# Performance work log

Measured on AMD Instinct MI355X. Metric: run time of the kernel, lower is better.

The kernel has to match this reference:

```python
import jax, jax.numpy as jnp
import numpy as np

K = 20  # kNN neighbours (conf.k)

def knn_edge_feats(x, k):
    """x: [B, C, N] -> edge features [B, 2C, N, k] (central || neighbor-central)."""
    xt = jnp.swapaxes(x, 1, 2)                       # [B, N, C]
    sq = jnp.sum(xt * xt, axis=2, keepdims=True)     # [B, N, 1]
    dist = -2.0 * jnp.einsum('bnc,bcm->bnm', xt, x) + sq + jnp.swapaxes(sq, 1, 2)  # [B,N,N]
    idx = jnp.argsort(dist, axis=2)[:, :, 1:k + 1]   # [B, N, k], skip self (col 0)
    nbrs = jax.vmap(lambda xb, ib: xb[:, ib])(x, idx)  # [B, C, N, k]
    central = x[:, :, :, None]                        # [B, C, N, 1]
    return jnp.concatenate([jnp.broadcast_to(central, nbrs.shape), nbrs - central], axis=1)

def edge_conv(x, w, b, k):
    """1x1 conv over edge features, max over k.  x:[B,C,N], w:[Fout,2C], b:[Fout]."""
    ee = knn_edge_feats(x, k)                                   # [B, 2C, N, k]
    y = jnp.einsum('oc,bcnk->bonk', w, ee) + b[None, :, None, None]
    return jnp.max(y, axis=3)                                   # [B, Fout, N]

def setup_inputs() -> dict:
    key = jax.random.key(0)
    ks = iter(jax.random.split(key, 32))
    B, N = 16, 2048
    d = {}
    d['x'] = jax.random.normal(next(ks), (B, 3, N), dtype=jnp.float32)
    def w(shape, scale):
        return jax.random.normal(next(ks), shape, dtype=jnp.float32) * scale
    d['ec0_w'] = w((64, 6), 0.3);    d['ec0_b'] = w((64,), 0.05)
    d['ec1_w'] = w((64, 128), 0.08); d['ec1_b'] = w((64,), 0.05)
    d['ec2_w'] = w((64, 128), 0.08); d['ec2_b'] = w((64,), 0.05)
    d['ec3_w'] = w((128, 128), 0.08); d['ec3_b'] = w((128,), 0.05)
    d['conv0_w'] = w((1024, 320), 0.05); d['conv0_b'] = w((1024,), 0.05)
    d['conv0_s'] = jax.random.uniform(next(ks), (1024,), minval=0.5, maxval=1.5)
    d['conv0_t'] = w((1024,), 0.05)
    d['fc0_w'] = w((512, 1024), 0.03); d['fc0_b'] = w((512,), 0.05)
    d['fc0_s'] = jax.random.uniform(next(ks), (512,), minval=0.5, maxval=1.5)
    d['fc0_t'] = w((512,), 0.05)
    d['fc1_w'] = w((256, 512), 0.04); d['fc1_b'] = w((256,), 0.05)
    d['fc1_s'] = jax.random.uniform(next(ks), (256,), minval=0.5, maxval=1.5)
    d['fc1_t'] = w((256,), 0.05)
    d['fc2_w'] = w((40, 256), 0.06); d['fc2_b'] = w((40,), 0.05)
    d['fc2_s'] = jax.random.uniform(next(ks), (40,), minval=0.5, maxval=1.5)
    d['fc2_t'] = w((40,), 0.05)
    return d

def reference(x, ec0_w, ec0_b, ec1_w, ec1_b, ec2_w, ec2_b, ec3_w, ec3_b,
              conv0_w, conv0_b, conv0_s, conv0_t,
              fc0_w, fc0_b, fc0_s, fc0_t,
              fc1_w, fc1_b, fc1_s, fc1_t,
              fc2_w, fc2_b, fc2_s, fc2_t):
    x1 = edge_conv(x, ec0_w, ec0_b, K)    # [B, 64, N]
    x2 = edge_conv(x1, ec1_w, ec1_b, K)   # [B, 64, N]
    x3 = edge_conv(x2, ec2_w, ec2_b, K)   # [B, 64, N]
    x4 = edge_conv(x3, ec3_w, ec3_b, K)   # [B, 128, N]
    h = jnp.concatenate([x1, x2, x3, x4], axis=1)              # [B, 320, N]
    # conv1dbr: 1x1 conv + BN(affine folded into s,t) + ReLU
    h = jnp.einsum('oc,bcn->bon', conv0_w, h) + conv0_b[None, :, None]
    h = jax.nn.relu(h * conv0_s[None, :, None] + conv0_t[None, :, None])  # [B, 1024, N]
    g = jnp.max(h, axis=2)                                     # [B, 1024]
    # fcbr blocks: linear + BN + ReLU
    g = jax.nn.relu((g @ fc0_w.T + fc0_b) * fc0_s + fc0_t)     # [B, 512]
    g = jax.nn.relu((g @ fc1_w.T + fc1_b) * fc1_s + fc1_t)     # [B, 256]
    g = jax.nn.relu((g @ fc2_w.T + fc2_b) * fc2_s + fc2_t)     # [B, 40]
    return g
```

## Files before the change

### kernel.cpp

```cpp
#include <hip/hip_runtime.h>

#define DEVINL __device__ __forceinline__

static const int NPTS = 2048;

typedef __attribute__((ext_vector_type(8))) short bf16x8;
typedef __attribute__((ext_vector_type(4))) float f32x4;

DEVINL unsigned fenc(float x) {
    int b = __float_as_int(x);
    return (b < 0) ? ~(unsigned)b : ((unsigned)b | 0x80000000u);
}
DEVINL float fdec(unsigned u) {
    return (u & 0x80000000u) ? __int_as_float((int)(u & 0x7fffffffu))
                             : __int_as_float((int)~u);
}
DEVINL unsigned long long u64min(unsigned long long a, unsigned long long b) {
    return (b < a) ? b : a;
}
DEVINL unsigned short f2bf(float x) {
    unsigned u = __float_as_uint(x);
    return (unsigned short)((u + 0x7fffu + ((u >> 16) & 1u)) >> 16);
}
DEVINL float bf2f(unsigned short h) { return __uint_as_float(((unsigned)h) << 16); }

DEVINL void topk20(float v[32], unsigned long long* cand, int lane,
                   int* __restrict__ Iout, int outBase) {
    float t16[16];
#pragma unroll
    for (int i = 0; i < 16; ++i) t16[i] = fminf(v[i], v[i + 16]);
#pragma unroll
    for (int i = 0; i < 8; ++i) t16[i] = fminf(t16[i], t16[i + 8]);
#pragma unroll
    for (int i = 0; i < 4; ++i) t16[i] = fminf(t16[i], t16[i + 4]);
    float s = fminf(fminf(t16[0], t16[1]), fminf(t16[2], t16[3]));
#pragma unroll
    for (int k = 2; k <= 64; k <<= 1) {
#pragma unroll
        for (int j = k >> 1; j >= 1; j >>= 1) {
            float o = __shfl_xor(s, j);
            bool keepmin = (((lane & j) == 0) == ((lane & k) == 0));
            s = keepmin ? fminf(s, o) : fmaxf(s, o);
        }
    }
    const float tau = __shfl(s, 19);
    int cnt = 0;
#pragma unroll
    for (int j = 0; j < 32; ++j) {
        bool pass = (v[j] <= tau);
        unsigned long long mask = __ballot(pass);
        if (pass) {
            int pos = cnt + (int)__popcll(mask & ((1ull << lane) - 1ull));
            if (pos < 64) {
                int col = lane * 4 + (j & 3) + ((j >> 2) << 8);
                cand[pos] = ((unsigned long long)fenc(v[j]) << 32) | (unsigned)col;
            }
        }
        cnt += (int)__popcll(mask);
    }
    if (cnt <= 64) {
        unsigned long long key = (lane < cnt) ? cand[lane] : ~0ull;
#pragma unroll
        for (int k = 2; k <= 64; k <<= 1) {
#pragma unroll
            for (int j = k >> 1; j >= 1; j >>= 1) {
                unsigned long long o = __shfl_xor(key, j);
                bool keepmin = (((lane & j) == 0) == ((lane & k) == 0));
                unsigned long long mn = u64min(key, o);
                unsigned long long mx = (key ^ o) ^ mn;
                key = keepmin ? mn : mx;
            }
        }
        if (lane < 20) Iout[outBase + lane] = (int)(unsigned)(key & 0xffffffffu);
    } else {
        unsigned long long vk[32];
#pragma unroll
        for (int j = 0; j < 32; ++j) {
            int col = lane * 4 + (j & 3) + ((j >> 2) << 8);
            vk[j] = ((unsigned long long)fenc(v[j]) << 32) | (unsigned)col;
        }
        unsigned long long last = 0ull;
        for (int it = 0; it < 20; ++it) {
            unsigned long long q16[16];
#pragma unroll
            for (int i = 0; i < 16; ++i) {
                unsigned long long a = (vk[i] > last) ? vk[i] : ~0ull;
                unsigned long long c = (vk[i + 16] > last) ? vk[i + 16] : ~0ull;
                q16[i] = u64min(a, c);
            }
#pragma unroll
            for (int i = 0; i < 8; ++i) q16[i] = u64min(q16[i], q16[i + 8]);
#pragma unroll
            for (int i = 0; i < 4; ++i) q16[i] = u64min(q16[i], q16[i + 4]);
            unsigned long long best = u64min(u64min(q16[0], q16[1]), u64min(q16[2], q16[3]));
#pragma unroll
            for (int off = 32; off >= 1; off >>= 1) {
                unsigned long long o = __shfl_down(best, off);
                best = u64min(best, o);
            }
            best = __shfl(best, 0);
            if (lane == 0) Iout[outBase + it] = (int)(unsigned)(best & 0xffffffffu);
            last = best;
        }
    }
}

__global__ __launch_bounds__(256) void sqmax_kernel(const float* __restrict__ X, int bs,
                                                    float* __restrict__ sqOut,
                                                    unsigned* __restrict__ Rsq) {
    const int N = NPTS;
    const int b = blockIdx.y, m = blockIdx.x * 256 + threadIdx.x;
    const float* __restrict__ Xb = X + (size_t)b * bs;
    float s = 0.f;
#pragma unroll 8
    for (int c = 0; c < 64; ++c) { float t = Xb[(size_t)c * N + m]; s = fmaf(t, t, s); }
    sqOut[(b << 11) + m] = s;
    float mx = s;
#pragma unroll
    for (int off = 32; off >= 1; off >>= 1) mx = fmaxf(mx, __shfl_down(mx, off));
    if ((threadIdx.x & 63) == 0) atomicMax(&Rsq[b], __float_as_uint(mx));
}

__global__ __launch_bounds__(512) void knnmfma_kernel(
    const unsigned short* __restrict__ HtH, const unsigned short* __restrict__ HtL,
    int hoff, const float* __restrict__ Xt,
    const float* __restrict__ sqB, const unsigned* __restrict__ Rsq,
    int* __restrict__ Iout) {
    extern __shared__ char smem[];
    float* Dr = (float*)smem;
    int* cand = (int*)(smem + 65792);
    const int N = NPTS, K = 20, DS = 1028;
    const int b = blockIdx.y, n0 = blockIdx.x * 16;
    const int tid = threadIdx.x, wave = tid >> 6, lane = tid & 63;
    const int fr = lane & 15, quad = lane >> 4;
    const float Rmax = sqrtf(__uint_as_float(Rsq[b]));

    const size_t abase = ((size_t)(b * N + n0 + fr)) * 320 + hoff + quad * 8;
    const bf16x8 aH0 = *(const bf16x8*)&HtH[abase];
    const bf16x8 aH1 = *(const bf16x8*)&HtH[abase + 32];
    const bf16x8 aL0 = *(const bf16x8*)&HtL[abase];
    const bf16x8 aL1 = *(const bf16x8*)&HtL[abase + 32];

    float v[2][2][16];
#pragma unroll
    for (int pass = 0; pass < 2; ++pass) {
#pragma unroll 2
        for (int tt = 0; tt < 8; ++tt) {
            const int m0 = pass * 1024 + wave * 128 + tt * 16;
            const size_t bbase = ((size_t)(b * N + m0 + fr)) * 320 + hoff + quad * 8;
            bf16x8 bH0 = *(const bf16x8*)&HtH[bbase];
            bf16x8 bH1 = *(const bf16x8*)&HtH[bbase + 32];
            bf16x8 bL0 = *(const bf16x8*)&HtL[bbase];
            bf16x8 bL1 = *(const bf16x8*)&HtL[bbase + 32];
            f32x4 acc = (f32x4){0.f, 0.f, 0.f, 0.f};
            acc = __builtin_amdgcn_mfma_f32_16x16x32_bf16(aH0, bH0, acc, 0, 0, 0);
            acc = __builtin_amdgcn_mfma_f32_16x16x32_bf16(aH1, bH1, acc, 0, 0, 0);
            acc = __builtin_amdgcn_mfma_f32_16x16x32_bf16(aH0, bL0, acc, 0, 0, 0);
            acc = __builtin_amdgcn_mfma_f32_16x16x32_bf16(aH1, bL1, acc, 0, 0, 0);
            acc = __builtin_amdgcn_mfma_f32_16x16x32_bf16(aL0, bH0, acc, 0, 0, 0);
            acc = __builtin_amdgcn_mfma_f32_16x16x32_bf16(aL1, bH1, acc, 0, 0, 0);
            const float sqv = sqB[(b << 11) + m0 + fr];
            const int mloc = wave * 128 + tt * 16 + fr;
#pragma unroll
            for (int r = 0; r < 4; ++r)
                Dr[(quad * 4 + r) * DS + mloc] = sqv - 2.f * acc[r];
        }
        __syncthreads();
#pragma unroll
        for (int rr = 0; rr < 2; ++rr) {
            const float* __restrict__ rp = &Dr[(wave * 2 + rr) * DS];
#pragma unroll
            for (int q = 0; q < 4; ++q) {
                float4 x4 = *(const float4*)&rp[lane * 4 + q * 256];
                v[pass][rr][q * 4 + 0] = x4.x; v[pass][rr][q * 4 + 1] = x4.y;
                v[pass][rr][q * 4 + 2] = x4.z; v[pass][rr][q * 4 + 3] = x4.w;
            }
        }
        __syncthreads();
    }

    int cntk[2];
#pragma unroll
    for (int rr = 0; rr < 2; ++rr) {
        const int nrow = n0 + wave * 2 + rr;
        float lm = v[0][rr][0];
#pragma unroll
        for (int j = 1; j < 16; ++j) lm = fminf(lm, v[0][rr][j]);
#pragma unroll
        for (int j = 0; j < 16; ++j) lm = fminf(lm, v[1][rr][j]);
        float s = lm;
#pragma unroll
        for (int k = 2; k <= 64; k <<= 1) {
#pragma unroll
            for (int j = k >> 1; j >= 1; j >>= 1) {
                float o = __shfl_xor(s, j);
                bool keepmin = (((lane & j) == 0) == ((lane & k) == 0));
                s = keepmin ? fminf(s, o) : fmaxf(s, o);
            }
        }
        const float tau21 = __shfl(s, 20);
        const float sqn = sqB[(b << 11) + nrow];
        const float margin = 3e-4f * sqrtf(fmaxf(sqn, 0.f)) * Rmax + 1e-12f;
        const float cutoff = tau21 + 2.f * margin;
        int cnt = 0;
        int* cl = &cand[(wave * 2 + rr) * 64];
#pragma unroll
        for (int pass = 0; pass < 2; ++pass) {
#pragma unroll
            for (int j = 0; j < 16; ++j) {
                bool p = (v[pass][rr][j] <= cutoff);
                unsigned long long mask = __ballot(p);
                if (p) {
                    int pos = cnt + (int)__popcll(mask & ((1ull << lane) - 1ull));
                    if (pos < 64)
                        cl[pos] = pass * 1024 + lane * 4 + (j & 3) + ((j >> 2) << 8);
                }
                cnt += (int)__popcll(mask);
            }
        }
        cntk[rr] = (cnt > 64) ? 64 : cnt;
    }

#pragma unroll 1
    for (int rr = 0; rr < 2; ++rr) {
        const int nrow = n0 + wave * 2 + rr;
        const int cnt = cntk[rr];
        const float* __restrict__ xn = &Xt[((size_t)(b * N + nrow)) << 6];
        unsigned long long key = ~0ull;
        if (lane < cnt) {
            const int m = cand[(wave * 2 + rr) * 64 + lane];
            const float* __restrict__ xm = &Xt[((size_t)(b * N + m)) << 6];
            float acc = 0.f;
#pragma unroll
            for (int q = 0; q < 16; ++q) {
                float4 a4 = *(const float4*)&xn[q * 4];
                float4 b4 = *(const float4*)&xm[q * 4];
                acc = fmaf(a4.x, b4.x, acc);
                acc = fmaf(a4.y, b4.y, acc);
                acc = fmaf(a4.z, b4.z, acc);
                acc = fmaf(a4.w, b4.w, acc);
            }
            const float d = sqB[(b << 11) + m] - 2.f * acc;
            key = ((unsigned long long)fenc(d) << 32) | (unsigned)m;
        }
#pragma unroll
        for (int k = 2; k <= 64; k <<= 1) {
#pragma unroll
            for (int j = k >> 1; j >= 1; j >>= 1) {
                unsigned long long o = __shfl_xor(key, j);
                bool keepmin = (((lane & j) == 0) == ((lane & k) == 0));
                unsigned long long mn = u64min(key, o);
                key = keepmin ? mn : ((key ^ o) ^ mn);
            }
        }
        if (lane >= 1 && lane < 21)
            Iout[(b * N + nrow) * K + (lane - 1)] = (int)(unsigned)(key & 0xffffffffu);
    }
}

__global__ __launch_bounds__(256) void select0_kernel(const float* __restrict__ X,
                                                      int* __restrict__ Iout) {
    const int N = NPTS, K = 20;
    __shared__ unsigned long long cand[4][64];
    const int w = threadIdx.x >> 6, lane = threadIdx.x & 63;
    const int rowg = blockIdx.x * 4 + w;
    const int b = rowg >> 11, n = rowg & 2047;
    const float* __restrict__ Xb = X + (size_t)b * 3 * N;
    const float xr = Xb[n], yr = Xb[N + n], zr = Xb[2 * N + n];
    const float INF = __builtin_inff();
    float v[32];
#pragma unroll
    for (int q = 0; q < 8; ++q) {
        const int base = lane * 4 + q * 256;
        const float4 xm = *(const float4*)&Xb[base];
        const float4 ym = *(const float4*)&Xb[N + base];
        const float4 zm = *(const float4*)&Xb[2 * N + base];
        float mx[4] = {xm.x, xm.y, xm.z, xm.w};
        float my[4] = {ym.x, ym.y, ym.z, ym.w};
        float mz[4] = {zm.x, zm.y, zm.z, zm.w};
#pragma unroll
        for (int j = 0; j < 4; ++j) {
            float sq = mx[j] * mx[j] + my[j] * my[j] + mz[j] * mz[j];
            float dot = xr * mx[j] + yr * my[j] + zr * mz[j];
            float d = sq - 2.f * dot;
            v[q * 4 + j] = (base + j == n) ? INF : d;
        }
    }
    topk20(v, &cand[w][0], lane, Iout, (b * N + n) * K);
}

template<int F, int C>
__global__ __launch_bounds__(256) void ut_kernel(const float* __restrict__ X, int bs,
                                                 const float* __restrict__ W,
                                                 const float* __restrict__ bias,
                                                 float* __restrict__ U, float* __restrict__ T) {
    const int N = NPTS;
    __shared__ float Ws2[64][C + 1];
    __shared__ float Wsd[64][C + 1];
    const int n0 = blockIdx.x * 64, f0 = blockIdx.y * 64, b = blockIdx.z;
    const int tid = threadIdx.x;
    for (int i = tid; i < 64 * C; i += 256) {
        int ff = i / C, c = i - ff * C;
        float w1 = W[(f0 + ff) * (2 * C) + c];
        float w2 = W[(f0 + ff) * (2 * C) + C + c];
        Ws2[ff][c] = w2;
        Wsd[ff][c] = w1 - w2;
    }
    __syncthreads();
    const int nt = tid & 15, fg = tid >> 4;
    const float* __restrict__ Xb = X + (size_t)b * bs;
    float au[4][4], av[4][4];
#pragma unroll
    for (int i = 0; i < 4; ++i)
#pragma unroll
        for (int j = 0; j < 4; ++j) { au[i][j] = 0.f; av[i][j] = 0.f; }
#pragma unroll 4
    for (int c = 0; c < C; ++c) {
        const float4 xv = *(const float4*)&Xb[(size_t)c * N + n0 + nt * 4];
#pragma unroll
        for (int fi = 0; fi < 4; ++fi) {
            float w2v = Ws2[fg * 4 + fi][c];
            float wdv = Wsd[fg * 4 + fi][c];
            au[fi][0] += w2v * xv.x; au[fi][1] += w2v * xv.y;
            au[fi][2] += w2v * xv.z; au[fi][3] += w2v * xv.w;
            av[fi][0] += wdv * xv.x; av[fi][1] += wdv * xv.y;
            av[fi][2] += wdv * xv.z; av[fi][3] += wdv * xv.w;
        }
    }
#pragma unroll
    for (int ni = 0; ni < 4; ++ni) {
        int n = n0 + nt * 4 + ni;
        float4 uv = make_float4(au[0][ni], au[1][ni], au[2][ni], au[3][ni]);
        *(float4*)&U[((size_t)b * N + n) * F + f0 + fg * 4] = uv;
    }
#pragma unroll
    for (int fi = 0; fi < 4; ++fi) {
        int f = f0 + fg * 4 + fi;
        float bv = bias[f];
        float4 tv = make_float4(av[fi][0] + bv, av[fi][1] + bv, av[fi][2] + bv, av[fi][3] + bv);
        *(float4*)&T[((size_t)b * F + f) * N + n0 + nt * 4] = tv;
    }
}

template<int F, bool WRITE_F32, bool WRITE_XT>
__global__ __launch_bounds__(256) void gathermax_kernel(const float* __restrict__ U,
                                                        const float* __restrict__ T,
                                                        const int* __restrict__ idx,
                                                        float* __restrict__ Y, int bsY,
                                                        unsigned short* __restrict__ HtH,
                                                        unsigned short* __restrict__ HtL,
                                                        int hoff,
                                                        float* __restrict__ Xt) {
    const int N = NPTS, K = 20, FG = F / 8;
    __shared__ int sidx[32 * 20];
    const int b = blockIdx.y, n0 = blockIdx.x * 32, tid = threadIdx.x;
    const int p = tid >> 3, fg = tid & 7;
    for (int t = tid; t < 32 * K; t += 256) sidx[t] = idx[(b * N + n0) * K + t];
    __syncthreads();
    const int n = n0 + p;
    const float* __restrict__ Ub = U + (size_t)b * N * F;
    const int fbase = fg * FG;
    float mx[FG];
#pragma unroll
    for (int i = 0; i < FG; ++i) mx[i] = -__builtin_inff();
#pragma unroll 4
    for (int j = 0; j < K; ++j) {
        const int r = sidx[p * K + j];
        const float4* up = (const float4*)&Ub[(size_t)r * F + fbase];
#pragma unroll
        for (int q = 0; q < FG / 4; ++q) {
            float4 a = up[q];
            mx[q * 4 + 0] = fmaxf(mx[q * 4 + 0], a.x);
            mx[q * 4 + 1] = fmaxf(mx[q * 4 + 1], a.y);
            mx[q * 4 + 2] = fmaxf(mx[q * 4 + 2], a.z);
            mx[q * 4 + 3] = fmaxf(mx[q * 4 + 3], a.w);
        }
    }
    float val[FG];
#pragma unroll
    for (int i = 0; i < FG; ++i) {
        const int f = fbase + i;
        val[i] = T[((size_t)b * F + f) * N + n] + mx[i];
        if (WRITE_F32) Y[(size_t)b * bsY + (size_t)f * N + n] = val[i];
    }
    if (WRITE_XT) {
        float* xp = &Xt[(((size_t)(b * N + n)) << 6) + fbase];
#pragma unroll
        for (int q = 0; q < FG / 4; ++q)
            *(float4*)&xp[q * 4] = *(const float4*)&val[q * 4];
    }
    unsigned short hs[FG], ls[FG];
#pragma unroll
    for (int i = 0; i < FG; ++i) {
        unsigned short h = f2bf(val[i]);
        hs[i] = h;
        ls[i] = f2bf(val[i] - bf2f(h));
    }
    const size_t hb = ((size_t)b * N + n) * 320 + hoff + fbase;
#pragma unroll
    for (int q = 0; q < FG / 8; ++q) {
        *(int4*)&HtH[hb + q * 8] = *(const int4*)&hs[q * 8];
        *(int4*)&HtL[hb + q * 8] = *(const int4*)&ls[q * 8];
    }
}

__global__ __launch_bounds__(256) void wsplit_kernel(const float* __restrict__ W,
                                                     unsigned short* __restrict__ WH,
                                                     unsigned short* __restrict__ WL) {
    const int e = blockIdx.x * 256 + threadIdx.x;
    float w = W[e];
    unsigned short h = f2bf(w);
    WH[e] = h;
    WL[e] = f2bf(w - bf2f(h));
}

__global__ __launch_bounds__(256) void conv0mfma_kernel(const unsigned short* __restrict__ HtH,
                                                        const unsigned short* __restrict__ HtL,
                                                        const unsigned short* __restrict__ WH,
                                                        const unsigned short* __restrict__ WL,
                                                        unsigned* __restrict__ M) {
    const int N = NPTS;
    __shared__ unsigned short HsH[64][40], HsL[64][40], WsH[128][40], WsL[128][40];
    const int n0 = blockIdx.x * 64, f0 = blockIdx.y * 128, b = blockIdx.z;
    const int tid = threadIdx.x;
    const int wave = tid >> 6, lane = tid & 63;
    const int wm = wave & 1, wf = wave >> 1;
    const int row = lane & 15, quad = lane >> 4;
    f32x4 acc[2][4];
#pragma unroll
    for (int i = 0; i < 2; ++i)
#pragma unroll
        for (int j = 0; j < 4; ++j) acc[i][j] = (f32x4){0.f, 0.f, 0.f, 0.f};

    const int hn = tid >> 2, hq = tid & 3;
    const int wfr = tid >> 1, wq = tid & 1;

    for (int c0 = 0; c0 < 320; c0 += 32) {
        {
            const size_t src = ((size_t)b * N + n0 + hn) * 320 + c0 + hq * 8;
            *(int4*)&HsH[hn][hq * 8] = *(const int4*)&HtH[src];
            *(int4*)&HsL[hn][hq * 8] = *(const int4*)&HtL[src];
        }
        {
            const size_t src = (size_t)(f0 + wfr) * 320 + c0 + wq * 16;
            *(int4*)&WsH[wfr][wq * 16]     = *(const int4*)&WH[src];
            *(int4*)&WsH[wfr][wq * 16 + 8] = *(const int4*)&WH[src + 8];
            *(int4*)&WsL[wfr][wq * 16]     = *(const int4*)&WL[src];
            *(int4*)&WsL[wfr][wq * 16 + 8] = *(const int4*)&WL[src + 8];
        }
        __syncthreads();
        bf16x8 aH[2], aL[2];
#pragma unroll
        for (int mt = 0; mt < 2; ++mt) {
            aH[mt] = *(const bf16x8*)&HsH[wm * 32 + mt * 16 + row][quad * 8];
            aL[mt] = *(const bf16x8*)&HsL[wm * 32 + mt * 16 + row][quad * 8];
        }
#pragma unroll
        for (int nt = 0; nt < 4; ++nt) {
            bf16x8 bH = *(const bf16x8*)&WsH[wf * 64 + nt * 16 + row][quad * 8];
            bf16x8 bL = *(const bf16x8*)&WsL[wf * 64 + nt * 16 + row][quad * 8];
#pragma unroll
            for (int mt = 0; mt < 2; ++mt) {
                acc[mt][nt] = __builtin_amdgcn_mfma_f32_16x16x32_bf16(aH[mt], bH, acc[mt][nt], 0, 0, 0);
                acc[mt][nt] = __builtin_amdgcn_mfma_f32_16x16x32_bf16(aH[mt], bL, acc[mt][nt], 0, 0, 0);
                acc[mt][nt] = __builtin_amdgcn_mfma_f32_16x16x32_bf16(aL[mt], bH, acc[mt][nt], 0, 0, 0);
            }
        }
        __syncthreads();
    }
#pragma unroll
    for (int nt = 0; nt < 4; ++nt) {
        float m = acc[0][nt][0];
#pragma unroll
        for (int r = 1; r < 4; ++r) m = fmaxf(m, acc[0][nt][r]);
#pragma unroll
        for (int r = 0; r < 4; ++r) m = fmaxf(m, acc[1][nt][r]);
        m = fmaxf(m, __shfl_down(m, 16));
        m = fmaxf(m, __shfl_down(m, 32));
        if (quad == 0)
            atomicMax(&M[(b << 10) + f0 + wf * 64 + nt * 16 + row], fenc(m));
    }
}

__global__ __launch_bounds__(256) void fc_kernel(const unsigned* __restrict__ M,
    const float* __restrict__ cb, const float* __restrict__ cs, const float* __restrict__ ct,
    const float* __restrict__ w0, const float* __restrict__ b0, const float* __restrict__ s0, const float* __restrict__ t0,
    const float* __restrict__ w1, const float* __restrict__ b1, const float* __restrict__ s1, const float* __restrict__ t1,
    const float* __restrict__ w2, const float* __restrict__ b2, const float* __restrict__ s2, const float* __restrict__ t2,
    float* __restrict__ out) {
    __shared__ float g0[1024], g1[512], g2[256];
    const int b = blockIdx.x, tid = threadIdx.x;
    for (int f = tid; f < 1024; f += 256) {
        float z = fdec(M[b * 1024 + f]);
        float g = cs[f] * (z + cb[f]) + ct[f];
        g0[f] = fmaxf(g, 0.f);
    }
    __syncthreads();
    for (int f = tid; f < 512; f += 256) {
        const float4* wp = (const float4*)(w0 + (size_t)f * 1024);
        float acc = 0.f;
#pragma unroll 4
        for (int c = 0; c < 256; ++c) {
            float4 wv = wp[c];
            float4 gv = *(const float4*)&g0[c * 4];
            acc += wv.x * gv.x + wv.y * gv.y + wv.z * gv.z + wv.w * gv.w;
        }
        float g = s0[f] * (acc + b0[f]) + t0[f];
        g1[f] = fmaxf(g, 0.f);
    }
    __syncthreads();
    if (tid < 256) {
        const float4* wp = (const float4*)(w1 + (size_t)tid * 512);
        float acc = 0.f;
#pragma unroll 4
        for (int c = 0; c < 128; ++c) {
            float4 wv = wp[c];
            float4 gv = *(const float4*)&g1[c * 4];
            acc += wv.x * gv.x + wv.y * gv.y + wv.z * gv.z + wv.w * gv.w;
        }
        float g = s1[tid] * (acc + b1[tid]) + t1[tid];
        g2[tid] = fmaxf(g, 0.f);
    }
    __syncthreads();
    if (tid < 40) {
        const float4* wp = (const float4*)(w2 + (size_t)tid * 256);
        float acc = 0.f;
#pragma unroll 4
        for (int c = 0; c < 64; ++c) {
            float4 wv = wp[c];
            float4 gv = *(const float4*)&g2[c * 4];
            acc += wv.x * gv.x + wv.y * gv.y + wv.z * gv.z + wv.w * gv.w;
        }
        float g = s2[tid] * (acc + b2[tid]) + t2[tid];
        out[b * 40 + tid] = fmaxf(g, 0.f);
    }
}

extern "C" void kernel_launch(void* const* d_in, const int* in_sizes, int n_in,
                              void* d_out, int out_size, void* d_ws, size_t ws_size,
                              hipStream_t stream) {
    const float* x       = (const float*)d_in[0];
    const float* ec0_w   = (const float*)d_in[1];
    const float* ec0_b   = (const float*)d_in[2];
    const float* ec1_w   = (const float*)d_in[3];
    const float* ec1_b   = (const float*)d_in[4];
    const float* ec2_w   = (const float*)d_in[5];
    const float* ec2_b   = (const float*)d_in[6];
    const float* ec3_w   = (const float*)d_in[7];
    const float* ec3_b   = (const float*)d_in[8];
    const float* conv0_w = (const float*)d_in[9];
    const float* conv0_b = (const float*)d_in[10];
    const float* conv0_s = (const float*)d_in[11];
    const float* conv0_t = (const float*)d_in[12];
    const float* fc0_w   = (const float*)d_in[13];
    const float* fc0_b   = (const float*)d_in[14];
    const float* fc0_s   = (const float*)d_in[15];
    const float* fc0_t   = (const float*)d_in[16];
    const float* fc1_w   = (const float*)d_in[17];
    const float* fc1_b   = (const float*)d_in[18];
    const float* fc1_s   = (const float*)d_in[19];
    const float* fc1_t   = (const float*)d_in[20];
    const float* fc2_w   = (const float*)d_in[21];
    const float* fc2_b   = (const float*)d_in[22];
    const float* fc2_s   = (const float*)d_in[23];
    const float* fc2_t   = (const float*)d_in[24];
    float* out = (float*)d_out;

    char* ws = (char*)d_ws;
    const int B = 16, N = NPTS;
    float* Hc   = (float*)(ws + 0);
    float* U    = (float*)(ws + 41943040);
    float* T    = (float*)(ws + 58720256);
    int*   I    = (int*)  (ws + 75497472);
    unsigned* M = (unsigned*)(ws + 78118912);
    unsigned short* W_hi = (unsigned short*)(ws + 78184448);
    unsigned short* W_lo = (unsigned short*)(ws + 78839808);
    unsigned short* HtH  = (unsigned short*)(ws + 79495168);
    unsigned short* HtL  = (unsigned short*)(ws + 100466688);
    float* sqb  = (float*)(ws + 121438208);
    unsigned* Rsq = (unsigned*)(ws + 121569280);
    float* Xt   = (float*)(ws + 121569344);

    (void)hipFuncSetAttribute((const void*)knnmfma_kernel,
                              hipFuncAttributeMaxDynamicSharedMemorySize, 69888);

    dim3 blk(256);
    const int bsX0 = 3 * N, bsH = 320 * N;

    wsplit_kernel<<<dim3(1024 * 320 / 256), blk, 0, stream>>>(conv0_w, W_hi, W_lo);

    select0_kernel<<<dim3(B * N / 4), blk, 0, stream>>>(x, I);
    ut_kernel<64, 3><<<dim3(N / 64, 1, B), blk, 0, stream>>>(x, bsX0, ec0_w, ec0_b, U, T);
    gathermax_kernel<64, true, true><<<dim3(N / 32, B), blk, 0, stream>>>(
        U, T, I, Hc, bsH, HtH, HtL, 0, Xt);

    const float* Xin[3] = {Hc, Hc + (size_t)64 * N, Hc + (size_t)128 * N};
    const float* ecw[3] = {ec1_w, ec2_w, ec3_w};
    const float* ecb[3] = {ec1_b, ec2_b, ec3_b};
    for (int L = 0; L < 3; ++L) {
        (void)hipMemsetAsync(Rsq, 0, B * sizeof(unsigned), stream);
        sqmax_kernel<<<dim3(N / 256, B), blk, 0, stream>>>(Xin[L], bsH, sqb, Rsq);
        knnmfma_kernel<<<dim3(N / 16, B), dim3(512), 69888, stream>>>(
            HtH, HtL, 64 * L, Xt, sqb, Rsq, I);
        if (L < 2) {
            ut_kernel<64, 64><<<dim3(N / 64, 1, B), blk, 0, stream>>>(Xin[L], bsH, ecw[L], ecb[L], U, T);
            gathermax_kernel<64, true, true><<<dim3(N / 32, B), blk, 0, stream>>>(
                U, T, I, Hc + (size_t)(64 * (L + 1)) * N, bsH, HtH, HtL, 64 * (L + 1), Xt);
        } else {
            ut_kernel<128, 64><<<dim3(N / 64, 2, B), blk, 0, stream>>>(Xin[L], bsH, ecw[L], ecb[L], U, T);
            gathermax_kernel<128, false, false><<<dim3(N / 32, B), blk, 0, stream>>>(
                U, T, I, Hc + (size_t)192 * N, bsH, HtH, HtL, 192, Xt);
        }
    }

    (void)hipMemsetAsync(M, 0, B * 1024 * sizeof(unsigned), stream);
    conv0mfma_kernel<<<dim3(N / 64, 1024 / 128, B), blk, 0, stream>>>(HtH, HtL, W_hi, W_lo, M);

    fc_kernel<<<dim3(B), blk, 0, stream>>>(M, conv0_b, conv0_s, conv0_t,
                                           fc0_w, fc0_b, fc0_s, fc0_t,
                                           fc1_w, fc1_b, fc1_s, fc1_t,
                                           fc2_w, fc2_b, fc2_s, fc2_t, out);
}
```

Before: 1.058 ms.

## Restructure kNN MFMA kernel: 32-row tiles, bf16 distance staging, wider candidate refinement

The kNN distance kernel now handles 32 query rows per block with 1024 threads, so each loaded B fragment feeds two MFMA accumulator sets. The coarse distance matrix is staged in shared memory as bf16 instead of fp32, which cuts LDS footprint and allows static shared memory and four passes. The running row minimum is computed during staging, and the candidate list grows from 64 to 96, refined exactly with a two-stage bitonic merge. Block IDs are remapped to interleave batches. The costs are a looser cutoff margin to absorb bf16 rounding, more candidates to refine exactly, and a risk of missing true neighbours if the margin is too tight.

Result: slower. 1.141 ms (+7.8%).

```diff
diff --git a/kernel.cpp b/kernel.cpp
--- a/kernel.cpp
+++ b/kernel.cpp
@@ -23,6 +23,22 @@
     return (unsigned short)((u + 0x7fffu + ((u >> 16) & 1u)) >> 16);
 }
 DEVINL float bf2f(unsigned short h) { return __uint_as_float(((unsigned)h) << 16); }
+DEVINL float bfLo(unsigned u) { return __uint_as_float(u << 16); }
+DEVINL float bfHi(unsigned u) { return __uint_as_float(u & 0xffff0000u); }
+
+DEVINL unsigned long long bitonic64(unsigned long long key, int lane) {
+#pragma unroll
+    for (int k = 2; k <= 64; k <<= 1) {
+#pragma unroll
+        for (int j = k >> 1; j >= 1; j >>= 1) {
+            unsigned long long o = __shfl_xor(key, j);
+            bool keepmin = (((lane & j) == 0) == ((lane & k) == 0));
+            unsigned long long mn = u64min(key, o);
+            key = keepmin ? mn : ((key ^ o) ^ mn);
+        }
+    }
+    return key;
+}
 
 DEVINL void topk20(float v[32], unsigned long long* cand, int lane,
                    int* __restrict__ Iout, int outBase) {
@@ -60,17 +76,7 @@
     }
     if (cnt <= 64) {
         unsigned long long key = (lane < cnt) ? cand[lane] : ~0ull;
-#pragma unroll
-        for (int k = 2; k <= 64; k <<= 1) {
-#pragma unroll
-            for (int j = k >> 1; j >= 1; j >>= 1) {
-                unsigned long long o = __shfl_xor(key, j);
-                bool keepmin = (((lane & j) == 0) == ((lane & k) == 0));
-                unsigned long long mn = u64min(key, o);
-                unsigned long long mx = (key ^ o) ^ mn;
-                key = keepmin ? mn : mx;
-            }
-        }
+        key = bitonic64(key, lane);
         if (lane < 20) Iout[outBase + lane] = (int)(unsigned)(key & 0xffffffffu);
     } else {
         unsigned long long vk[32];
@@ -121,74 +127,88 @@
     if ((threadIdx.x & 63) == 0) atomicMax(&Rsq[b], __float_as_uint(mx));
 }
 
-__global__ __launch_bounds__(512) void knnmfma_kernel(
+__global__ __launch_bounds__(1024) void knnmfma_kernel(
     const unsigned short* __restrict__ HtH, const unsigned short* __restrict__ HtL,
     int hoff, const float* __restrict__ Xt,
     const float* __restrict__ sqB, const unsigned* __restrict__ Rsq,
     int* __restrict__ Iout) {
-    extern __shared__ char smem[];
-    float* Dr = (float*)smem;
-    int* cand = (int*)(smem + 65792);
-    const int N = NPTS, K = 20, DS = 1028;
-    const int b = blockIdx.y, n0 = blockIdx.x * 16;
+    __shared__ unsigned short Dr[32 * 524];
+    __shared__ int cand[32 * 96];
+    const int N = NPTS, K = 20, DS = 524;
+    const int id = blockIdx.x;
+    const int b = (id & 7) + 8 * ((id >> 3) & 1);
+    const int n0 = (id >> 4) * 32;
     const int tid = threadIdx.x, wave = tid >> 6, lane = tid & 63;
     const int fr = lane & 15, quad = lane >> 4;
     const float Rmax = sqrtf(__uint_as_float(Rsq[b]));
-
-    const size_t abase = ((size_t)(b * N + n0 + fr)) * 320 + hoff + quad * 8;
-    const bf16x8 aH0 = *(const bf16x8*)&HtH[abase];
-    const bf16x8 aH1 = *(const bf16x8*)&HtH[abase + 32];
-    const bf16x8 aL0 = *(const bf16x8*)&HtL[abase];
-    const bf16x8 aL1 = *(const bf16x8*)&HtL[abase + 32];
-
-    float v[2][2][16];
-#pragma unroll
-    for (int pass = 0; pass < 2; ++pass) {
-#pragma unroll 2
-        for (int tt = 0; tt < 8; ++tt) {
-            const int m0 = pass * 1024 + wave * 128 + tt * 16;
-            const size_t bbase = ((size_t)(b * N + m0 + fr)) * 320 + hoff + quad * 8;
+    const float INF = __builtin_inff();
+
+    bf16x8 aH[2][2], aL[2][2];
+#pragma unroll
+    for (int t = 0; t < 2; ++t) {
+        const size_t abase = ((size_t)(b * N + n0 + t * 16 + fr)) * 320 + hoff + quad * 8;
+        aH[t][0] = *(const bf16x8*)&HtH[abase];
+        aH[t][1] = *(const bf16x8*)&HtH[abase + 32];
+        aL[t][0] = *(const bf16x8*)&HtL[abase];
+        aL[t][1] = *(const bf16x8*)&HtL[abase + 32];
+    }
+
+    const int rowA = wave * 2;
+    unsigned vv[2][4][4];
+    float lmin[2] = {INF, INF};
+
+#pragma unroll 1
+    for (int pass = 0; pass < 4; ++pass) {
+#pragma unroll
+        for (int tt = 0; tt < 2; ++tt) {
+            const int mloc = wave * 32 + tt * 16 + fr;
+            const int m = pass * 512 + mloc;
+            const size_t bbase = ((size_t)(b * N + m)) * 320 + hoff + quad * 8;
             bf16x8 bH0 = *(const bf16x8*)&HtH[bbase];
             bf16x8 bH1 = *(const bf16x8*)&HtH[bbase + 32];
             bf16x8 bL0 = *(const bf16x8*)&HtL[bbase];
             bf16x8 bL1 = *(const bf16x8*)&HtL[bbase + 32];
-            f32x4 acc = (f32x4){0.f, 0.f, 0.f, 0.f};
-            acc = __builtin_amdgcn_mfma_f32_16x16x32_bf16(aH0, bH0, acc, 0, 0, 0);
-            acc = __builtin_amdgcn_mfma_f32_16x16x32_bf16(aH1, bH1, acc, 0, 0, 0);
-            acc = __builtin_amdgcn_mfma_f32_16x16x32_bf16(aH0, bL0, acc, 0, 0, 0);
-            acc = __builtin_amdgcn_mfma_f32_16x16x32_bf16(aH1, bL1, acc, 0, 0, 0);
-            acc = __builtin_amdgcn_mfma_f32_16x16x32_bf16(aL0, bH0, acc, 0, 0, 0);
-            acc = __builtin_amdgcn_mfma_f32_16x16x32_bf16(aL1, bH1, acc, 0, 0, 0);
-            const float sqv = sqB[(b << 11) + m0 + fr];
-            const int mloc = wave * 128 + tt * 16 + fr;
-#pragma unroll
-            for (int r = 0; r < 4; ++r)
-                Dr[(quad * 4 + r) * DS + mloc] = sqv - 2.f * acc[r];
+            f32x4 a0 = (f32x4){0.f, 0.f, 0.f, 0.f};
+            f32x4 a1 = (f32x4){0.f, 0.f, 0.f, 0.f};
+            a0 = __builtin_amdgcn_mfma_f32_16x16x32_bf16(aH[0][0], bH0, a0, 0, 0, 0);
+            a0 = __builtin_amdgcn_mfma_f32_16x16x32_bf16(aH[0][1], bH1, a0, 0, 0, 0);
+            a0 = __builtin_amdgcn_mfma_f32_16x16x32_bf16(aH[0][0], bL0, a0, 0, 0, 0);
+            a0 = __builtin_amdgcn_mfma_f32_16x16x32_bf16(aH[0][1], bL1, a0, 0, 0, 0);
+            a0 = __builtin_amdgcn_mfma_f32_16x16x32_bf16(aL[0][0], bH0, a0, 0, 0, 0);
+            a0 = __builtin_amdgcn_mfma_f32_16x16x32_bf16(aL[0][1], bH1, a0, 0, 0, 0);
+            a1 = __builtin_amdgcn_mfma_f32_16x16x32_bf16(aH[1][0], bH0, a1, 0, 0, 0);
+            a1 = __builtin_amdgcn_mfma_f32_16x16x32_bf16(aH[1][1], bH1, a1, 0, 0, 0);
+            a1 = __builtin_amdgcn_mfma_f32_16x16x32_bf16(aH[1][0], bL0, a1, 0, 0, 0);
+            a1 = __builtin_amdgcn_mfma_f32_16x16x32_bf16(aH[1][1], bL1, a1, 0, 0, 0);
+            a1 = __builtin_amdgcn_mfma_f32_16x16x32_bf16(aL[1][0], bH0, a1, 0, 0, 0);
+            a1 = __builtin_amdgcn_mfma_f32_16x16x32_bf16(aL[1][1], bH1, a1, 0, 0, 0);
+            const float sqv = sqB[(b << 11) + m];
+#pragma unroll
+            for (int r = 0; r < 4; ++r) {
+                Dr[(quad * 4 + r) * DS + mloc]        = f2bf(sqv - 2.f * a0[r]);
+                Dr[(16 + quad * 4 + r) * DS + mloc]   = f2bf(sqv - 2.f * a1[r]);
+            }
         }
         __syncthreads();
 #pragma unroll
         for (int rr = 0; rr < 2; ++rr) {
-            const float* __restrict__ rp = &Dr[(wave * 2 + rr) * DS];
-#pragma unroll
-            for (int q = 0; q < 4; ++q) {
-                float4 x4 = *(const float4*)&rp[lane * 4 + q * 256];
-                v[pass][rr][q * 4 + 0] = x4.x; v[pass][rr][q * 4 + 1] = x4.y;
-                v[pass][rr][q * 4 + 2] = x4.z; v[pass][rr][q * 4 + 3] = x4.w;
-            }
+            const int row = rowA + rr;
+            uint2 p0 = *(const uint2*)&Dr[row * DS + lane * 4];
+            uint2 p1 = *(const uint2*)&Dr[row * DS + lane * 4 + 256];
+            vv[rr][pass][0] = p0.x; vv[rr][pass][1] = p0.y;
+            vv[rr][pass][2] = p1.x; vv[rr][pass][3] = p1.y;
+            float m0 = fminf(fminf(bfLo(p0.x), bfHi(p0.x)), fminf(bfLo(p0.y), bfHi(p0.y)));
+            float m1 = fminf(fminf(bfLo(p1.x), bfHi(p1.x)), fminf(bfLo(p1.y), bfHi(p1.y)));
+            lmin[rr] = fminf(lmin[rr], fminf(m0, m1));
         }
         __syncthreads();
     }
 
     int cntk[2];
-#pragma unroll
+#pragma unroll 1
     for (int rr = 0; rr < 2; ++rr) {
-        const int nrow = n0 + wave * 2 + rr;
-        float lm = v[0][rr][0];
-#pragma unroll
-        for (int j = 1; j < 16; ++j) lm = fminf(lm, v[0][rr][j]);
-#pragma unroll
-        for (int j = 0; j < 16; ++j) lm = fminf(lm, v[1][rr][j]);
-        float s = lm;
+        const int nrow = n0 + rowA + rr;
+        float s = lmin[rr];
 #pragma unroll
         for (int k = 2; k <= 64; k <<= 1) {
 #pragma unroll
@@ -200,35 +220,40 @@
         }
         const float tau21 = __shfl(s, 20);
         const float sqn = sqB[(b << 11) + nrow];
-        const float margin = 3e-4f * sqrtf(fmaxf(sqn, 0.f)) * Rmax + 1e-12f;
-        const float cutoff = tau21 + 2.f * margin;
+        const float margin = 3e-4f * sqrtf(fmaxf(sqn, 0.f)) * Rmax;
+        const float cutoff = tau21 + 2.02f * margin + 0.005f * fabsf(tau21) + 1e-6f;
         int cnt = 0;
-        int* cl = &cand[(wave * 2 + rr) * 64];
-#pragma unroll
-        for (int pass = 0; pass < 2; ++pass) {
-#pragma unroll
-            for (int j = 0; j < 16; ++j) {
-                bool p = (v[pass][rr][j] <= cutoff);
-                unsigned long long mask = __ballot(p);
-                if (p) {
-                    int pos = cnt + (int)__popcll(mask & ((1ull << lane) - 1ull));
-                    if (pos < 64)
-                        cl[pos] = pass * 1024 + lane * 4 + (j & 3) + ((j >> 2) << 8);
+        int* cl = &cand[(rowA + rr) * 96];
+#pragma unroll
+        for (int pass = 0; pass < 4; ++pass) {
+#pragma unroll
+            for (int g = 0; g < 4; ++g) {
+#pragma unroll
+                for (int h = 0; h < 2; ++h) {
+                    float val = h ? bfHi(vv[rr][pass][g]) : bfLo(vv[rr][pass][g]);
+                    bool p = (val <= cutoff);
+                    unsigned long long mask = __ballot(p);
+                    if (p) {
+                        int pos = cnt + (int)__popcll(mask & ((1ull << lane) - 1ull));
+                        if (pos < 96)
+                            cl[pos] = pass * 512 + (g >> 1) * 256 + lane * 4 + (g & 1) * 2 + h;
+                    }
+                    cnt += (int)__popcll(mask);
                 }
-                cnt += (int)__popcll(mask);
-            }
-        }
-        cntk[rr] = (cnt > 64) ? 64 : cnt;
+            }
+        }
+        cntk[rr] = (cnt > 96) ? 96 : cnt;
     }
 
 #pragma unroll 1
     for (int rr = 0; rr < 2; ++rr) {
-        const int nrow = n0 + wave * 2 + rr;
+        const int nrow = n0 + rowA + rr;
         const int cnt = cntk[rr];
+        const int* cl = &cand[(rowA + rr) * 96];
         const float* __restrict__ xn = &Xt[((size_t)(b * N + nrow)) << 6];
-        unsigned long long key = ~0ull;
-        if (lane < cnt) {
-            const int m = cand[(wave * 2 + rr) * 64 + lane];
+        unsigned long long kA = ~0ull;
+        if (lane < cnt && lane < 64) {
+            const int m = cl[lane];
             const float* __restrict__ xm = &Xt[((size_t)(b * N + m)) << 6];
             float acc = 0.f;
 #pragma unroll
@@ -241,20 +266,36 @@
                 acc = fmaf(a4.w, b4.w, acc);
             }
             const float d = sqB[(b << 11) + m] - 2.f * acc;
-            key = ((unsigned long long)fenc(d) << 32) | (unsigned)m;
-        }
-#pragma unroll
-        for (int k = 2; k <= 64; k <<= 1) {
-#pragma unroll
-            for (int j = k >> 1; j >= 1; j >>= 1) {
-                unsigned long long o = __shfl_xor(key, j);
-                bool keepmin = (((lane & j) == 0) == ((lane & k) == 0));
-                unsigned long long mn = u64min(key, o);
-                key = keepmin ? mn : ((key ^ o) ^ mn);
-            }
+            kA = ((unsigned long long)fenc(d) << 32) | (unsigned)m;
+        }
+        kA = bitonic64(kA, lane);
+        unsigned long long kOut = kA;
+        if (cnt > 64) {
+            unsigned long long kB = ~0ull;
+            if (lane < cnt - 64) {
+                const int m = cl[64 + lane];
+                const float* __restrict__ xm = &Xt[((size_t)(b * N + m)) << 6];
+                float acc = 0.f;
+#pragma unroll
+                for (int q = 0; q < 16; ++q) {
+                    float4 a4 = *(const float4*)&xn[q * 4];
+                    float4 b4 = *(const float4*)&xm[q * 4];
+                    acc = fmaf(a4.x, b4.x, acc);
+                    acc = fmaf(a4.y, b4.y, acc);
+                    acc = fmaf(a4.z, b4.z, acc);
+                    acc = fmaf(a4.w, b4.w, acc);
+                }
+                const float d = sqB[(b << 11) + m] - 2.f * acc;
+                kB = ((unsigned long long)fenc(d) << 32) | (unsigned)m;
+            }
+            kB = bitonic64(kB, lane);
+            unsigned long long kb = __shfl(kB, lane - 32);
+            unsigned long long key = (lane < 21) ? kA
+                                   : (lane >= 32 && lane < 53) ? kb : ~0ull;
+            kOut = bitonic64(key, lane);
         }
         if (lane >= 1 && lane < 21)
-            Iout[(b * N + nrow) * K + (lane - 1)] = (int)(unsigned)(key & 0xffffffffu);
+            Iout[(b * N + nrow) * K + (lane - 1)] = (int)(unsigned)(kOut & 0xffffffffu);
     }
 }
 
@@ -581,9 +622,6 @@
     unsigned* Rsq = (unsigned*)(ws + 121569280);
     float* Xt   = (float*)(ws + 121569344);
 
-    (void)hipFuncSetAttribute((const void*)knnmfma_kernel,
-                              hipFuncAttributeMaxDynamicSharedMemorySize, 69888);
-
     dim3 blk(256);
     const int bsX0 = 3 * N, bsH = 320 * N;
 
@@ -600,7 +638,7 @@
     for (int L = 0; L < 3; ++L) {
         (void)hipMemsetAsync(Rsq, 0, B * sizeof(unsigned), stream);
         sqmax_kernel<<<dim3(N / 256, B), blk, 0, stream>>>(Xin[L], bsH, sqb, Rsq);
-        knnmfma_kernel<<<dim3(N / 16, B), dim3(512), 69888, stream>>>(
+        knnmfma_kernel<<<dim3(1024), dim3(1024), 0, stream>>>(
             HtH, HtL, 64 * L, Xt, sqb, Rsq, I);
         if (L < 2) {
             ut_kernel<64, 64><<<dim3(N / 64, 1, B), blk, 0, stream>>>(Xin[L], bsH, ecw[L], ecb[L], U, T);
```
